# Kernel optimization log

Measured on AMD Instinct MI355X. Metric: run time of the kernel, lower is better.

Reference implementation:

```python
import math
import jax, jax.numpy as jnp
import numpy as np

B, S, H, NH, HD = 2, 1024, 5120, 40, 128

def _get_interleave(n):
    def _pow2(n):
        start = 2 ** (-2 ** (-(math.log2(n) - 3)))
        return [start * start ** i for i in range(n)]
    if math.log2(n).is_integer():
        return _pow2(n)
    cp2 = 2 ** math.floor(math.log2(n))
    return _pow2(cp2) + _get_interleave(2 * cp2)[0::2][: n - cp2]

def _gen_alibi_mask(n_head, max_pos):
    # Baichuan's ALiBi: bias[h, i, j] = slope_h * j  + (-inf if j > i else 0)
    # (slope_h * j is equivalent to slope_h * (j - i) up to a per-row constant)
    slopes = np.asarray(_get_interleave(n_head), dtype=np.float32)  # [H]
    pos = np.arange(max_pos, dtype=np.float32)                       # j
    alibi = slopes[:, None, None] * pos[None, None, :]               # [H,1,M]
    tri = np.triu(np.full((max_pos, max_pos), -np.inf, dtype=np.float32), 1)
    return tri[None, :, :] + alibi                                   # [H,M,M]

def setup_inputs() -> dict:
    key = jax.random.key(0)
    k1, k2, k3 = jax.random.split(key, 3)
    hidden_states = jax.random.normal(k1, (B, S, H), dtype=jnp.float32)
    attention_mask = jnp.asarray(_gen_alibi_mask(NH, S))              # [40,1024,1024]
    W_pack = jax.random.normal(k2, (3 * H, H), dtype=jnp.float32) * 0.02
    o_proj = jax.random.normal(k3, (H, H), dtype=jnp.float32) * 0.02
    return {"hidden_states": hidden_states, "attention_mask": attention_mask,
            "W_pack": W_pack, "o_proj": o_proj}

def reference(hidden_states, attention_mask, W_pack, o_proj):
    bsz, q_len, hid = hidden_states.shape
    n_heads, head_dim = NH, hid // NH
    # fused QKV projection (torch linear: x @ W^T)
    proj = jnp.einsum('bsh,oh->bso', hidden_states, W_pack)          # [B,S,3H]
    q, k, v = jnp.split(proj, 3, axis=-1)
    def to_heads(t):
        return t.reshape(bsz, q_len, n_heads, head_dim).transpose(0, 2, 1, 3)
    q, k, v = to_heads(q), to_heads(k), to_heads(v)                  # [B,NH,S,D]
    scores = jnp.einsum('bhqd,bhkd->bhqk', q, k) / math.sqrt(head_dim)
    scores = scores + attention_mask                                 # broadcast [NH,S,S]
    scores = jnp.maximum(scores, jnp.finfo(scores.dtype).min)        # clamp like torch
    probs = jax.nn.softmax(scores, axis=-1)
    attn = jnp.einsum('bhqk,bhkd->bhqd', probs, v)                   # [B,NH,S,D]
    attn = attn.transpose(0, 2, 1, 3).reshape(bsz, q_len, hid)
    return jnp.einsum('bsh,oh->bso', attn, o_proj)
```

## Files before the change

kernel.cpp:

```cpp
#include <hip/hip_runtime.h>

#define NHEADS 40
#define HDIM 128
#define SEQ 1024
#define HID 5120
#define KDIM 5120
#define NEG_BIG (-1e30f)

typedef unsigned short u16;
typedef unsigned int u32;
typedef __attribute__((ext_vector_type(8))) short s16x8;
typedef __attribute__((ext_vector_type(4))) float fx4;

__device__ __forceinline__ u32 f2bf_rne(float f) {
    const u32 u = __float_as_uint(f);
    return (u + 0x7fffu + ((u >> 16) & 1u)) >> 16;
}

__global__ void split_bf16(const float* __restrict__ X, u16* __restrict__ Hh,
                           u16* __restrict__ Ll, long n8) {
    const long stride = (long)gridDim.x * blockDim.x;
    for (long i = (long)blockIdx.x * blockDim.x + threadIdx.x; i < n8; i += stride) {
        const float4 a = ((const float4*)X)[2 * i];
        const float4 b = ((const float4*)X)[2 * i + 1];
        const float f[8] = {a.x, a.y, a.z, a.w, b.x, b.y, b.z, b.w};
        u32 hw[8], lw[8];
#pragma unroll
        for (int j = 0; j < 8; ++j) {
            const u32 hb = f2bf_rne(f[j]);
            const float hf = __uint_as_float(hb << 16);
            hw[j] = hb;
            lw[j] = f2bf_rne(f[j] - hf);
        }
        uint4 ho, lo;
        ho.x = hw[0] | (hw[1] << 16); ho.y = hw[2] | (hw[3] << 16);
        ho.z = hw[4] | (hw[5] << 16); ho.w = hw[6] | (hw[7] << 16);
        lo.x = lw[0] | (lw[1] << 16); lo.y = lw[2] | (lw[3] << 16);
        lo.z = lw[4] | (lw[5] << 16); lo.w = lw[6] | (lw[7] << 16);
        ((uint4*)Hh)[i] = ho;
        ((uint4*)Ll)[i] = lo;
    }
}

__device__ __forceinline__ void gload_lds16(const void* g, void* l) {
    __builtin_amdgcn_global_load_lds(
        (const __attribute__((address_space(1))) void*)g,
        (__attribute__((address_space(3))) void*)l, 16, 0, 0);
}

template <int EPI>
__launch_bounds__(256, 2)
__global__ void gemm3_bt(const u16* __restrict__ Ah, const u16* __restrict__ Al,
                         const u16* __restrict__ Bh, const u16* __restrict__ Bl,
                         float* __restrict__ O0, float* __restrict__ O1,
                         float* __restrict__ O2) {
    __shared__ u16 sAh[4096], sAl[4096], sBh[4096], sBl[4096];

    const int t = threadIdx.x;
    const int lane = t & 63;
    const int w = t >> 6, wm = w >> 1, wn = w & 1;

    const int nwg = gridDim.x * gridDim.y;
    const int id = blockIdx.y * gridDim.x + blockIdx.x;
    const int v = (id & 7) * (nwg >> 3) + (id >> 3);
    const int nt = v >> 4, mt = v & 15;
    const int n0 = nt * 128, m0 = mt * 128;

    const int f0 = t, f1 = t + 256;
    const int r0 = f0 & 127, c0 = (f0 >> 7) * 8;
    const int r1 = f1 & 127, c1 = (f1 >> 7) * 8;
    const u16* gA0h = Ah + (long)(m0 + r0) * KDIM + c0;
    const u16* gA1h = Ah + (long)(m0 + r1) * KDIM + c1;
    const u16* gA0l = Al + (long)(m0 + r0) * KDIM + c0;
    const u16* gA1l = Al + (long)(m0 + r1) * KDIM + c1;
    const u16* gB0h = Bh + (long)(n0 + r0) * KDIM + c0;
    const u16* gB1h = Bh + (long)(n0 + r1) * KDIM + c1;
    const u16* gB0l = Bl + (long)(n0 + r0) * KDIM + c0;
    const u16* gB1l = Bl + (long)(n0 + r1) * KDIM + c1;
    u16* lA0h = &sAh[f0 * 8]; u16* lA1h = &sAh[f1 * 8];
    u16* lA0l = &sAl[f0 * 8]; u16* lA1l = &sAl[f1 * 8];
    u16* lB0h = &sBh[f0 * 8]; u16* lB1h = &sBh[f1 * 8];
    u16* lB0l = &sBl[f0 * 8]; u16* lB1l = &sBl[f1 * 8];

    const int kb = lane >> 4;
    const int offA = (kb * 128 + wm * 64 + (lane & 15)) * 8;
    const int offB = (kb * 128 + wn * 64 + (lane & 15)) * 8;

    fx4 acc[4][4] = {};

    for (int k0 = 0; k0 < KDIM; k0 += 32) {
        __syncthreads();
        gload_lds16(gA0h + k0, lA0h); gload_lds16(gA1h + k0, lA1h);
        gload_lds16(gA0l + k0, lA0l); gload_lds16(gA1l + k0, lA1l);
        gload_lds16(gB0h + k0, lB0h); gload_lds16(gB1h + k0, lB1h);
        gload_lds16(gB0l + k0, lB0l); gload_lds16(gB1l + k0, lB1l);
        __syncthreads();

        s16x8 avh[4], avl[4], bvh[4], bvl[4];
#pragma unroll
        for (int i = 0; i < 4; ++i) {
            avh[i] = *(const s16x8*)&sAh[offA + i * 128];
            avl[i] = *(const s16x8*)&sAl[offA + i * 128];
            bvh[i] = *(const s16x8*)&sBh[offB + i * 128];
            bvl[i] = *(const s16x8*)&sBl[offB + i * 128];
        }
#pragma unroll
        for (int mf = 0; mf < 4; ++mf)
#pragma unroll
            for (int nf = 0; nf < 4; ++nf) {
                fx4 c = acc[mf][nf];
                c = __builtin_amdgcn_mfma_f32_16x16x32_bf16(avh[mf], bvh[nf], c, 0, 0, 0);
                c = __builtin_amdgcn_mfma_f32_16x16x32_bf16(avh[mf], bvl[nf], c, 0, 0, 0);
                c = __builtin_amdgcn_mfma_f32_16x16x32_bf16(avl[mf], bvh[nf], c, 0, 0, 0);
                acc[mf][nf] = c;
            }
    }

    const int sec = (EPI == 0) ? (n0 / HID) : 0;
    float* Ob = (sec == 0) ? O0 : (sec == 1) ? O1 : O2;
    const int nsec0 = n0 - sec * HID;
#pragma unroll
    for (int mf = 0; mf < 4; ++mf) {
        const int mBase = m0 + wm * 64 + mf * 16 + (lane >> 4) * 4;
#pragma unroll
        for (int nf = 0; nf < 4; ++nf) {
            const int nn = nsec0 + wn * 64 + nf * 16 + (lane & 15);
#pragma unroll
            for (int r = 0; r < 4; ++r) {
                const int m = mBase + r;
                const float val = acc[mf][nf][r];
                if (EPI == 0) {
                    const int b = m >> 10, s = m & 1023;
                    const int h = nn >> 7, d = nn & 127;
                    Ob[(((long)(b * NHEADS + h)) * SEQ + s) * HDIM + d] = val;
                } else {
                    O0[(long)m * HID + nn] = val;
                }
            }
        }
    }
}

template <int EPI>
__launch_bounds__(256)
__global__ void gemm_bt(const float* __restrict__ A, const float* __restrict__ B,
                        float* __restrict__ O0, float* __restrict__ O1,
                        float* __restrict__ O2) {
    __shared__ float lA[32][132];
    __shared__ float lB[32][132];
    const int t = threadIdx.x;
    const int tm = t >> 4, tn = t & 15;
    const int m0 = blockIdx.y * 128, n0 = blockIdx.x * 128;
    const int sr = t >> 3;
    const int sk = (t & 7) * 4;

    float acc[8][8] = {};
    const float* Ag = A + (long)(m0 + sr) * KDIM + sk;
    const float* Bg = B + (long)(n0 + sr) * KDIM + sk;

    for (int k0 = 0; k0 < KDIM; k0 += 32) {
        __syncthreads();
#pragma unroll
        for (int p = 0; p < 4; ++p) {
            const float4 av = *(const float4*)(Ag + (long)p * 32 * KDIM + k0);
            const float4 bv = *(const float4*)(Bg + (long)p * 32 * KDIM + k0);
            const int m = sr + p * 32;
            lA[sk + 0][m] = av.x; lA[sk + 1][m] = av.y;
            lA[sk + 2][m] = av.z; lA[sk + 3][m] = av.w;
            lB[sk + 0][m] = bv.x; lB[sk + 1][m] = bv.y;
            lB[sk + 2][m] = bv.z; lB[sk + 3][m] = bv.w;
        }
        __syncthreads();
#pragma unroll 4
        for (int kk = 0; kk < 32; ++kk) {
            const float4 a0 = *(const float4*)&lA[kk][tm * 4];
            const float4 a1 = *(const float4*)&lA[kk][64 + tm * 4];
            const float4 b0 = *(const float4*)&lB[kk][tn * 4];
            const float4 b1 = *(const float4*)&lB[kk][64 + tn * 4];
            const float ar[8] = {a0.x, a0.y, a0.z, a0.w, a1.x, a1.y, a1.z, a1.w};
            const float br[8] = {b0.x, b0.y, b0.z, b0.w, b1.x, b1.y, b1.z, b1.w};
#pragma unroll
            for (int r = 0; r < 8; ++r)
#pragma unroll
                for (int c = 0; c < 8; ++c) acc[r][c] += ar[r] * br[c];
        }
    }

    const int sec = n0 / HID;
    const int h = (n0 % HID) / HDIM;
#pragma unroll
    for (int r8 = 0; r8 < 8; ++r8) {
        const int mi = m0 + ((r8 < 4) ? (tm * 4 + r8) : (64 + tm * 4 + (r8 - 4)));
        float4 v0, v1;
        v0.x = acc[r8][0]; v0.y = acc[r8][1]; v0.z = acc[r8][2]; v0.w = acc[r8][3];
        v1.x = acc[r8][4]; v1.y = acc[r8][5]; v1.z = acc[r8][6]; v1.w = acc[r8][7];
        if (EPI == 0) {
            const int b = mi >> 10, s = mi & 1023;
            float* Ob = (sec == 0) ? O0 : (sec == 1) ? O1 : O2;
            float* dst = Ob + ((long)(b * NHEADS + h) * SEQ + s) * HDIM;
            *(float4*)(dst + tn * 4) = v0;
            *(float4*)(dst + 64 + tn * 4) = v1;
        } else {
            float* dst = O0 + (long)mi * HID + n0;
            *(float4*)(dst + tn * 4) = v0;
            *(float4*)(dst + 64 + tn * 4) = v1;
        }
    }
}

__launch_bounds__(256)
__global__ void attn_fwd(const float* __restrict__ Q, const float* __restrict__ K,
                         const float* __restrict__ V, const float* __restrict__ mask,
                         float* __restrict__ ATT) {
    __shared__ float lQ[128][36];
    __shared__ float lK[128][36];
    __shared__ float lV[32][132];
    __shared__ float lP[32][36];
    __shared__ float lM[SEQ];

    const int t = threadIdx.x;
    const int tm = t >> 4, tn = t & 15;
    const int qt = blockIdx.x, h = blockIdx.y, b = blockIdx.z;
    const int q0 = qt * 32;
    const long bh = (long)b * NHEADS + h;
    const float* Qh = Q + bh * SEQ * HDIM;
    const float* Kh = K + bh * SEQ * HDIM;
    const float* Vh = V + bh * SEQ * HDIM;

    {
        const float* mrow = mask + ((long)h * SEQ + (SEQ - 1)) * SEQ;
#pragma unroll
        for (int p = 0; p < 4; ++p) {
            const int j = t + p * 256;
            lM[j] = fminf(fmaxf(mrow[j], NEG_BIG), 1e30f);
        }
    }
    {
        const int row = t >> 5;
        const int col = (t & 31) * 4;
#pragma unroll
        for (int p = 0; p < 4; ++p) {
            const float4 qv = *(const float4*)(Qh + (long)(q0 + row + p * 8) * HDIM + col);
            lQ[col + 0][row + p * 8] = qv.x; lQ[col + 1][row + p * 8] = qv.y;
            lQ[col + 2][row + p * 8] = qv.z; lQ[col + 3][row + p * 8] = qv.w;
        }
    }

    float O[2][8] = {};
    float mrun[2] = {NEG_BIG, NEG_BIG};
    float lrun[2] = {0.f, 0.f};
    const int i0 = q0 + tm * 2;
    const float scale = 0.08838834764831845f;

    __syncthreads();

    for (int kt = 0; kt <= qt; ++kt) {
        const int kv0 = kt * 32;
        if (kt) __syncthreads();
        {
            const int row = t >> 5;
            const int col = (t & 31) * 4;
#pragma unroll
            for (int p = 0; p < 4; ++p) {
                const float4 kv = *(const float4*)(Kh + (long)(kv0 + row + p * 8) * HDIM + col);
                lK[col + 0][row + p * 8] = kv.x; lK[col + 1][row + p * 8] = kv.y;
                lK[col + 2][row + p * 8] = kv.z; lK[col + 3][row + p * 8] = kv.w;
                const float4 vv = *(const float4*)(Vh + (long)(kv0 + row + p * 8) * HDIM + col);
                *(float4*)&lV[row + p * 8][col] = vv;
            }
        }
        __syncthreads();

        float S00 = 0.f, S01 = 0.f, S10 = 0.f, S11 = 0.f;
#pragma unroll 8
        for (int d = 0; d < 128; ++d) {
            const float2 qa = *(const float2*)&lQ[d][tm * 2];
            const float2 ka = *(const float2*)&lK[d][tn * 2];
            S00 += qa.x * ka.x; S01 += qa.x * ka.y;
            S10 += qa.y * ka.x; S11 += qa.y * ka.y;
        }
        float Sv[2][2] = {{S00, S01}, {S10, S11}};

        float tmax[2] = {NEG_BIG, NEG_BIG};
#pragma unroll
        for (int r = 0; r < 2; ++r)
#pragma unroll
            for (int c = 0; c < 2; ++c) {
                const int j = kv0 + tn * 2 + c;
                float vv = Sv[r][c] * scale + lM[j];
                if (j > i0 + r) vv = NEG_BIG;
                Sv[r][c] = vv;
                tmax[r] = fmaxf(tmax[r], vv);
            }
#pragma unroll
        for (int x = 1; x < 16; x <<= 1) {
            tmax[0] = fmaxf(tmax[0], __shfl_xor(tmax[0], x, 64));
            tmax[1] = fmaxf(tmax[1], __shfl_xor(tmax[1], x, 64));
        }
        float alpha[2], rsum[2] = {0.f, 0.f};
#pragma unroll
        for (int r = 0; r < 2; ++r) {
            const float mnew = fmaxf(mrun[r], tmax[r]);
            alpha[r] = __expf(mrun[r] - mnew);
            mrun[r] = mnew;
        }
#pragma unroll
        for (int r = 0; r < 2; ++r)
#pragma unroll
            for (int c = 0; c < 2; ++c) {
                const float pv = __expf(Sv[r][c] - mrun[r]);
                rsum[r] += pv;
                lP[tn * 2 + c][tm * 2 + r] = pv;
            }
#pragma unroll
        for (int x = 1; x < 16; x <<= 1) {
            rsum[0] += __shfl_xor(rsum[0], x, 64);
            rsum[1] += __shfl_xor(rsum[1], x, 64);
        }
#pragma unroll
        for (int r = 0; r < 2; ++r) lrun[r] = lrun[r] * alpha[r] + rsum[r];
#pragma unroll
        for (int dt = 0; dt < 8; ++dt) { O[0][dt] *= alpha[0]; O[1][dt] *= alpha[1]; }
        __syncthreads();

#pragma unroll 4
        for (int kv = 0; kv < 32; ++kv) {
            const float2 pf = *(const float2*)&lP[kv][tm * 2];
            const float4 va = *(const float4*)&lV[kv][tn * 8];
            const float4 vb = *(const float4*)&lV[kv][tn * 8 + 4];
            O[0][0] += pf.x * va.x; O[0][1] += pf.x * va.y;
            O[0][2] += pf.x * va.z; O[0][3] += pf.x * va.w;
            O[0][4] += pf.x * vb.x; O[0][5] += pf.x * vb.y;
            O[0][6] += pf.x * vb.z; O[0][7] += pf.x * vb.w;
            O[1][0] += pf.y * va.x; O[1][1] += pf.y * va.y;
            O[1][2] += pf.y * va.z; O[1][3] += pf.y * va.w;
            O[1][4] += pf.y * vb.x; O[1][5] += pf.y * vb.y;
            O[1][6] += pf.y * vb.z; O[1][7] += pf.y * vb.w;
        }
    }

    const float inv0 = 1.f / lrun[0], inv1 = 1.f / lrun[1];
    float* dst0 = ATT + (long)(b * SEQ + i0 + 0) * HID + h * HDIM + tn * 8;
    float* dst1 = ATT + (long)(b * SEQ + i0 + 1) * HID + h * HDIM + tn * 8;
    float4 o;
    o.x = O[0][0] * inv0; o.y = O[0][1] * inv0; o.z = O[0][2] * inv0; o.w = O[0][3] * inv0;
    *(float4*)dst0 = o;
    o.x = O[0][4] * inv0; o.y = O[0][5] * inv0; o.z = O[0][6] * inv0; o.w = O[0][7] * inv0;
    *(float4*)(dst0 + 4) = o;
    o.x = O[1][0] * inv1; o.y = O[1][1] * inv1; o.z = O[1][2] * inv1; o.w = O[1][3] * inv1;
    *(float4*)dst1 = o;
    o.x = O[1][4] * inv1; o.y = O[1][5] * inv1; o.z = O[1][6] * inv1; o.w = O[1][7] * inv1;
    *(float4*)(dst1 + 4) = o;
}

extern "C" void kernel_launch(void* const* d_in, const int* in_sizes, int n_in,
                              void* d_out, int out_size, void* d_ws, size_t ws_size,
                              hipStream_t stream) {
    const float* hid  = (const float*)d_in[0];
    const float* mask = (const float*)d_in[1];
    const float* wpk  = (const float*)d_in[2];
    const float* opr  = (const float*)d_in[3];
    float* out = (float*)d_out;

    const size_t SZF = (size_t)2 * NHEADS * SEQ * HDIM;
    const size_t EA = (size_t)2048 * 5120;
    const size_t EW = (size_t)5120 * 5120;
    char* ws = (char*)d_ws;
    float* Qb = (float*)ws;
    float* Kb = Qb + SZF;
    float* Vb = Kb + SZF;
    float* At = Vb + SZF;
    const size_t baseB = SZF * 4 * 4;
    u16* Ahh = (u16*)(ws + baseB);
    u16* Ahl = Ahh + EA;
    u16* Wh  = (u16*)(ws + baseB + 2 * EA * 2);

    const size_t needSec  = baseB + 2 * EA * 2 + 2 * EW * 2;
    const size_t needFull = baseB + 2 * EA * 2 + 6 * EW * 2;

    if (ws_size >= needSec) {
        const bool full = (ws_size >= needFull);
        split_bf16<<<1024, 256, 0, stream>>>(hid, Ahh, Ahl, (long)(EA / 8));
        if (full) {
            u16* Wl = Wh + 3 * EW;
            split_bf16<<<2048, 256, 0, stream>>>(wpk, Wh, Wl, (long)(3 * EW / 8));
            gemm3_bt<0><<<dim3(120, 16), 256, 0, stream>>>(Ahh, Ahl, Wh, Wl, Qb, Kb, Vb);
        } else {
            u16* Wl = Wh + EW;
            for (int s = 0; s < 3; ++s) {
                split_bf16<<<2048, 256, 0, stream>>>(wpk + s * EW, Wh, Wl, (long)(EW / 8));
                float* Ob = (s == 0) ? Qb : (s == 1) ? Kb : Vb;
                gemm3_bt<0><<<dim3(40, 16), 256, 0, stream>>>(Ahh, Ahl, Wh, Wl, Ob, Ob, Ob);
            }
        }
        attn_fwd<<<dim3(32, NHEADS, 2), 256, 0, stream>>>(Qb, Kb, Vb, mask, At);
        u16* Ath = Ahh; u16* Atl = Ahl;
        u16* Oph = Wh;  u16* Opl = Wh + EW;
        split_bf16<<<1024, 256, 0, stream>>>(At, Ath, Atl, (long)(EA / 8));
        split_bf16<<<2048, 256, 0, stream>>>(opr, Oph, Opl, (long)(EW / 8));
        gemm3_bt<1><<<dim3(40, 16), 256, 0, stream>>>(Ath, Atl, Oph, Opl, out,
                                                      nullptr, nullptr);
    } else {
        gemm_bt<0><<<dim3(120, 16), 256, 0, stream>>>(hid, wpk, Qb, Kb, Vb);
        attn_fwd<<<dim3(32, NHEADS, 2), 256, 0, stream>>>(Qb, Kb, Vb, mask, At);
        gemm_bt<1><<<dim3(40, 16), 256, 0, stream>>>(At, opr, out, nullptr, nullptr);
    }
}
```

Before: 4.348 ms.

## Double-buffer LDS tiles in split-bf16 GEMM to overlap loads with MFMA

Doubles the shared-memory staging buffers so the next K-slice is fetched with global_load_lds while MFMAs run on the current buffer, going from two barriers per iteration to one. It also raises wave priority around the MFMA block. LDS use doubles to 64KB per block, which may cut the two-blocks-per-CU occupancy. Correctness relies on the global_load_lds writes being complete before the single barrier, since no explicit vmcnt wait is added.

```diff
diff --git a/kernel.cpp b/kernel.cpp
--- a/kernel.cpp
+++ b/kernel.cpp
@@ -54,7 +54,7 @@
                          const u16* __restrict__ Bh, const u16* __restrict__ Bl,
                          float* __restrict__ O0, float* __restrict__ O1,
                          float* __restrict__ O2) {
-    __shared__ u16 sAh[4096], sAl[4096], sBh[4096], sBl[4096];
+    __shared__ u16 sAh[2][4096], sAl[2][4096], sBh[2][4096], sBl[2][4096];
 
     const int t = threadIdx.x;
     const int lane = t & 63;
@@ -77,10 +77,6 @@
     const u16* gB1h = Bh + (long)(n0 + r1) * KDIM + c1;
     const u16* gB0l = Bl + (long)(n0 + r0) * KDIM + c0;
     const u16* gB1l = Bl + (long)(n0 + r1) * KDIM + c1;
-    u16* lA0h = &sAh[f0 * 8]; u16* lA1h = &sAh[f1 * 8];
-    u16* lA0l = &sAl[f0 * 8]; u16* lA1l = &sAl[f1 * 8];
-    u16* lB0h = &sBh[f0 * 8]; u16* lB1h = &sBh[f1 * 8];
-    u16* lB0l = &sBl[f0 * 8]; u16* lB1l = &sBl[f1 * 8];
 
     const int kb = lane >> 4;
     const int offA = (kb * 128 + wm * 64 + (lane & 15)) * 8;
@@ -88,22 +84,35 @@
 
     fx4 acc[4][4] = {};
 
+#define STAGE3(buf, k0off) do {                                            \
+        gload_lds16(gA0h + (k0off), &sAh[buf][f0 * 8]);                    \
+        gload_lds16(gA1h + (k0off), &sAh[buf][f1 * 8]);                    \
+        gload_lds16(gA0l + (k0off), &sAl[buf][f0 * 8]);                    \
+        gload_lds16(gA1l + (k0off), &sAl[buf][f1 * 8]);                    \
+        gload_lds16(gB0h + (k0off), &sBh[buf][f0 * 8]);                    \
+        gload_lds16(gB1h + (k0off), &sBh[buf][f1 * 8]);                    \
+        gload_lds16(gB0l + (k0off), &sBl[buf][f0 * 8]);                    \
+        gload_lds16(gB1l + (k0off), &sBl[buf][f1 * 8]);                    \
+    } while (0)
+
+    STAGE3(0, 0);
+    __syncthreads();
+
+    int cur = 0;
     for (int k0 = 0; k0 < KDIM; k0 += 32) {
-        __syncthreads();
-        gload_lds16(gA0h + k0, lA0h); gload_lds16(gA1h + k0, lA1h);
-        gload_lds16(gA0l + k0, lA0l); gload_lds16(gA1l + k0, lA1l);
-        gload_lds16(gB0h + k0, lB0h); gload_lds16(gB1h + k0, lB1h);
-        gload_lds16(gB0l + k0, lB0l); gload_lds16(gB1l + k0, lB1l);
-        __syncthreads();
+        if (k0 + 32 < KDIM) {
+            if (cur == 0) STAGE3(1, k0 + 32); else STAGE3(0, k0 + 32);
+        }
 
         s16x8 avh[4], avl[4], bvh[4], bvl[4];
 #pragma unroll
         for (int i = 0; i < 4; ++i) {
-            avh[i] = *(const s16x8*)&sAh[offA + i * 128];
-            avl[i] = *(const s16x8*)&sAl[offA + i * 128];
-            bvh[i] = *(const s16x8*)&sBh[offB + i * 128];
-            bvl[i] = *(const s16x8*)&sBl[offB + i * 128];
-        }
+            avh[i] = *(const s16x8*)&sAh[cur][offA + i * 128];
+            avl[i] = *(const s16x8*)&sAl[cur][offA + i * 128];
+            bvh[i] = *(const s16x8*)&sBh[cur][offB + i * 128];
+            bvl[i] = *(const s16x8*)&sBl[cur][offB + i * 128];
+        }
+        __builtin_amdgcn_s_setprio(1);
 #pragma unroll
         for (int mf = 0; mf < 4; ++mf)
 #pragma unroll
@@ -114,7 +123,11 @@
                 c = __builtin_amdgcn_mfma_f32_16x16x32_bf16(avl[mf], bvh[nf], c, 0, 0, 0);
                 acc[mf][nf] = c;
             }
-    }
+        __builtin_amdgcn_s_setprio(0);
+        __syncthreads();
+        cur ^= 1;
+    }
+#undef STAGE3
 
     const int sec = (EPI == 0) ? (n0 / HID) : 0;
     float* Ob = (sec == 0) ? O0 : (sec == 1) ? O1 : O2;
```

New measurement: 4.134 ms. 4.9% less time.
